# Kernel optimization log

Measured on AMD Instinct MI355X. Metric: run time of the kernel, lower is better.

The kernel has to match this reference:

```python
import jax, jax.numpy as jnp
import numpy as np

EMBED_DIM = 1024
NUM_HEADS = 16
HEAD_DIM = EMBED_DIM // NUM_HEADS
B, S = 2, 2048


def setup_inputs() -> dict:
    key = jax.random.key(0)
    ks = jax.random.split(key, 11)
    sc = 1.0 / np.sqrt(EMBED_DIM)
    d = {
        'query': jax.random.normal(ks[0], (B, S, EMBED_DIM), jnp.float32),
        'key': jax.random.normal(ks[1], (B, S, EMBED_DIM), jnp.float32),
        'value': jax.random.normal(ks[2], (B, S, EMBED_DIM), jnp.float32),
        'Wq': jax.random.normal(ks[3], (EMBED_DIM, EMBED_DIM), jnp.float32) * sc,
        'bq': jnp.zeros((EMBED_DIM,), jnp.float32),
        'Wk': jax.random.normal(ks[4], (EMBED_DIM, EMBED_DIM), jnp.float32) * sc,
        'bk': jnp.zeros((EMBED_DIM,), jnp.float32),
        'Wv': jax.random.normal(ks[5], (EMBED_DIM, EMBED_DIM), jnp.float32) * sc,
        'bv': jnp.zeros((EMBED_DIM,), jnp.float32),
        'Wo': jax.random.normal(ks[6], (EMBED_DIM, EMBED_DIM), jnp.float32) * sc,
        'bo': jnp.zeros((EMBED_DIM,), jnp.float32),
    }
    return d


def reference(query, key, value, Wq, bq, Wk, bk, Wv, bv, Wo, bo):
    b, s, _ = query.shape
    scale = 1.0 / np.sqrt(HEAD_DIM)
    # projections: torch Linear is x @ W.T + b
    q = (query @ Wq.T + bq).reshape(b, s, NUM_HEADS, HEAD_DIM).transpose(0, 2, 1, 3)
    k = (key @ Wk.T + bk).reshape(b, s, NUM_HEADS, HEAD_DIM).transpose(0, 2, 1, 3)
    v = (value @ Wv.T + bv).reshape(b, s, NUM_HEADS, HEAD_DIM).transpose(0, 2, 1, 3)
    scores = jnp.einsum('bhqd,bhkd->bhqk', q, k) * scale  # [B,H,S,S]
    causal = jnp.triu(jnp.ones((s, s), bool), k=1)
    scores = jnp.where(causal, -jnp.inf, scores)
    attn = jax.nn.softmax(scores, axis=-1)
    out = jnp.einsum('bhqk,bhkd->bhqd', attn, v)
    out = out.transpose(0, 2, 1, 3).reshape(b, s, EMBED_DIM)
    out = out @ Wo.T + bo
    return out, attn
```

## Files before the change

kernel.cpp:

```cpp
#include <hip/hip_runtime.h>
#include <hip/hip_bf16.h>

#define BATCH  2
#define SEQ    2048
#define EMBED  1024
#define NHEADS 16
#define HDIM   64
#define SCALE  0.125f
#define S2     0.180336880f
#define MFIX   20.0f
#define PPITCH 88

typedef __attribute__((ext_vector_type(8))) short   short8;
typedef __attribute__((ext_vector_type(4))) float   floatx4;

#if __has_builtin(__builtin_amdgcn_exp2f)
#define EXP2(x) __builtin_amdgcn_exp2f(x)
#else
#define EXP2(x) exp2f(x)
#endif

#define GLOAD_LDS(g, l) __builtin_amdgcn_global_load_lds(                      \
    (const __attribute__((address_space(1))) void*)(const void*)(g),           \
    (__attribute__((address_space(3))) void*)(void*)(l), 16, 0, 0)

__device__ __forceinline__ float bf2f(unsigned short h) {
    union { unsigned int u; float f; } v; v.u = ((unsigned int)h) << 16; return v.f;
}
__device__ __forceinline__ unsigned short f2bf(float f) {
    union { float f; unsigned int u; } v; v.f = f;
    unsigned int r = v.u + 0x7FFF + ((v.u >> 16) & 1);
    return (unsigned short)(r >> 16);
}
__device__ __forceinline__ unsigned int pack2(float lo, float hi) {
    return (unsigned int)f2bf(lo) | ((unsigned int)f2bf(hi) << 16);
}

__device__ __forceinline__ void bar_lds() {
    __builtin_amdgcn_sched_barrier(0);
    asm volatile("s_waitcnt lgkmcnt(0)" ::: "memory");
    __builtin_amdgcn_s_barrier();
    __builtin_amdgcn_sched_barrier(0);
}

__global__ __launch_bounds__(256)
void cvt_bf16(const float* __restrict__ q,  const float* __restrict__ k,
              const float* __restrict__ v,  const float* __restrict__ wq,
              const float* __restrict__ wk, const float* __restrict__ wv,
              const float* __restrict__ wo,
              unsigned short* __restrict__ dq,  unsigned short* __restrict__ dk,
              unsigned short* __restrict__ dv,  unsigned short* __restrict__ dwq,
              unsigned short* __restrict__ dwk, unsigned short* __restrict__ dwv,
              unsigned short* __restrict__ dwo)
{
    const float* s; unsigned short* d; int n;
    switch (blockIdx.y) {
        case 0: s = q;  d = dq;  n = BATCH * SEQ * EMBED; break;
        case 1: s = k;  d = dk;  n = BATCH * SEQ * EMBED; break;
        case 2: s = v;  d = dv;  n = BATCH * SEQ * EMBED; break;
        case 3: s = wq; d = dwq; n = EMBED * EMBED; break;
        case 4: s = wk; d = dwk; n = EMBED * EMBED; break;
        case 5: s = wv; d = dwv; n = EMBED * EMBED; break;
        default: s = wo; d = dwo; n = EMBED * EMBED; break;
    }
    const int i = (blockIdx.x * 256 + threadIdx.x) * 8;
    if (i >= n) return;
    float4 f0 = ((const float4*)(s + i))[0];
    float4 f1 = ((const float4*)(s + i))[1];
    uint4 u = {pack2(f0.x, f0.y), pack2(f0.z, f0.w),
               pack2(f1.x, f1.y), pack2(f1.z, f1.w)};
    *(uint4*)(d + i) = u;
}

__device__ __forceinline__ void gemm_body(
    const unsigned short* __restrict__ A,
    const unsigned short* __restrict__ W,
    const float* __restrict__ bias,
    void* __restrict__ Cout, const int f32out)
{
    constexpr int N = EMBED;
    constexpr int K = EMBED;

    __shared__ unsigned short As[2][128 * 64];
    __shared__ unsigned short Bs[2][64 * 64];

    const int t    = threadIdx.x;
    const int w    = t >> 6;
    const int lane = t & 63;
    const int lr   = lane & 15;
    const int quad = lane >> 4;
    const int n0   = blockIdx.x * 64;
    const int m0   = blockIdx.y * 128;

    size_t agoff[4];
    #pragma unroll
    for (int i = 0; i < 4; ++i) {
        const int slot = i * 256 + w * 64 + lane;
        const int row  = slot >> 3;
        const int g    = (slot & 7) ^ (row & 7);
        agoff[i] = (size_t)(m0 + row) * K + g * 8;
    }
    size_t bgoff[2];
    #pragma unroll
    for (int i = 0; i < 2; ++i) {
        const int slot = i * 256 + w * 64 + lane;
        const int row  = slot >> 3;
        const int g    = (slot & 7) ^ (row & 7);
        bgoff[i] = (size_t)(n0 + row) * K + g * 8;
    }

    int aoff[2][2], boff[4][2];
    #pragma unroll
    for (int mb = 0; mb < 2; ++mb)
        #pragma unroll
        for (int s = 0; s < 2; ++s) {
            const int row = w * 32 + mb * 16 + lr;
            aoff[mb][s] = row * 64 + (((s * 4 + quad) ^ (row & 7)) * 8);
        }
    #pragma unroll
    for (int nb = 0; nb < 4; ++nb)
        #pragma unroll
        for (int s = 0; s < 2; ++s) {
            const int row = nb * 16 + lr;
            boff[nb][s] = row * 64 + (((s * 4 + quad) ^ (row & 7)) * 8);
        }

    floatx4 acc[2][4];
    #pragma unroll
    for (int mb = 0; mb < 2; ++mb)
        #pragma unroll
        for (int nb = 0; nb < 4; ++nb) acc[mb][nb] = (floatx4){0.f, 0.f, 0.f, 0.f};

    auto stage = [&](int buf, int k0) {
        #pragma unroll
        for (int i = 0; i < 4; ++i)
            GLOAD_LDS(A + agoff[i] + k0, &As[buf][(i * 256 + w * 64) * 8]);
        #pragma unroll
        for (int i = 0; i < 2; ++i)
            GLOAD_LDS(W + bgoff[i] + k0, &Bs[buf][(i * 256 + w * 64) * 8]);
    };
    auto compute = [&](int buf) {
        const unsigned short* Ab = As[buf];
        const unsigned short* Bb = Bs[buf];
        #pragma unroll
        for (int s = 0; s < 2; ++s) {
            short8 a0 = *(const short8*)&Ab[aoff[0][s]];
            short8 a1 = *(const short8*)&Ab[aoff[1][s]];
            #pragma unroll
            for (int nb = 0; nb < 4; ++nb) {
                short8 bfr = *(const short8*)&Bb[boff[nb][s]];
                acc[0][nb] = __builtin_amdgcn_mfma_f32_16x16x32_bf16(a0, bfr, acc[0][nb], 0, 0, 0);
                acc[1][nb] = __builtin_amdgcn_mfma_f32_16x16x32_bf16(a1, bfr, acc[1][nb], 0, 0, 0);
            }
        }
    };

    stage(0, 0);
    __syncthreads();
    for (int k0 = 0; k0 < K; k0 += 128) {
        if (k0 + 64 < K) stage(1, k0 + 64);
        compute(0);
        __syncthreads();
        if (k0 + 128 < K) stage(0, k0 + 128);
        compute(1);
        __syncthreads();
    }

    #pragma unroll
    for (int mb = 0; mb < 2; ++mb)
        #pragma unroll
        for (int nb = 0; nb < 4; ++nb) {
            const int col = n0 + nb * 16 + lr;
            const float bv = bias[col];
            #pragma unroll
            for (int r = 0; r < 4; ++r) {
                const int row = m0 + w * 32 + mb * 16 + quad * 4 + r;
                const float val = acc[mb][nb][r] + bv;
                if (f32out) ((float*)Cout)[(size_t)row * N + col] = val;
                else        ((unsigned short*)Cout)[(size_t)row * N + col] = f2bf(val);
            }
        }
}

__global__ __launch_bounds__(256)
void gemm_qkv(const unsigned short* __restrict__ xq, const unsigned short* __restrict__ xk,
              const unsigned short* __restrict__ xv,
              const unsigned short* __restrict__ wq, const unsigned short* __restrict__ wk,
              const unsigned short* __restrict__ wv,
              const float* __restrict__ bq, const float* __restrict__ bk,
              const float* __restrict__ bv,
              unsigned short* __restrict__ Qb, unsigned short* __restrict__ Kb,
              unsigned short* __restrict__ Vb)
{
    const unsigned short *A, *W; const float* bias; unsigned short* C;
    switch (blockIdx.z) {
        case 0:  A = xq; W = wq; bias = bq; C = Qb; break;
        case 1:  A = xk; W = wk; bias = bk; C = Kb; break;
        default: A = xv; W = wv; bias = bv; C = Vb; break;
    }
    gemm_body(A, W, bias, C, 0);
}

__global__ __launch_bounds__(256)
void gemm_out(const unsigned short* __restrict__ A, const unsigned short* __restrict__ W,
              const float* __restrict__ bias, float* __restrict__ Cout)
{
    gemm_body(A, W, bias, Cout, 1);
}

__global__ __launch_bounds__(256)
void attn_fused(const unsigned short* __restrict__ Qb,
                const unsigned short* __restrict__ Kb,
                const unsigned short* __restrict__ Vb,
                float* __restrict__ attn,
                unsigned short* __restrict__ AO)
{
    __shared__ unsigned short Ps[64][PPITCH];
    __shared__ unsigned short Vt[2][64][PPITCH];

    const int t    = threadIdx.x;
    const int w    = t >> 6;
    const int lane = t & 63;
    const int lr   = lane & 15;
    const int quad = lane >> 4;
    const int h    = blockIdx.y;
    const int b    = blockIdx.z;
    const int slot = (h >> 3) + 2 * b;
    const int qt   = (slot & 1) ? (SEQ / 64 - 1 - (int)blockIdx.x) : (int)blockIdx.x;
    const int q0   = qt * 64;
    const int srow = t >> 2;
    const int sseg = (t & 3) * 16;

    const size_t kvbase = (size_t)b * SEQ * EMBED + h * HDIM;

    const unsigned short* qrow = Qb + kvbase + (size_t)(q0 + w * 16 + lr) * EMBED + quad * 8;
    const short8 af0 = *(const short8*)(qrow);
    const short8 af1 = *(const short8*)(qrow + 32);

    const unsigned short* kfrag = Kb + kvbase + (size_t)lr * EMBED + quad * 8;
    const unsigned short* Vrow  = Vb + kvbase + (size_t)lane * EMBED;

    float lsum[4];
    #pragma unroll
    for (int r = 0; r < 4; ++r) lsum[r] = 0.f;

    for (int kt = 0; kt <= qt; ++kt) {
        const unsigned short* kp = kfrag + (size_t)(kt * 64) * EMBED;
        short8 kb0[4], kb1[4];
        #pragma unroll
        for (int nb = 0; nb < 4; ++nb) kb0[nb] = *(const short8*)(kp + (size_t)(nb * 16) * EMBED);
        #pragma unroll
        for (int nb = 0; nb < 4; ++nb) kb1[nb] = *(const short8*)(kp + (size_t)(nb * 16) * EMBED + 32);

        floatx4 sf[4];
        #pragma unroll
        for (int i = 0; i < 4; ++i) sf[i] = (floatx4){0.f, 0.f, 0.f, 0.f};
        #pragma unroll
        for (int nb = 0; nb < 4; ++nb)
            sf[nb] = __builtin_amdgcn_mfma_f32_16x16x32_bf16(af0, kb0[nb], sf[nb], 0, 0, 0);
        #pragma unroll
        for (int nb = 0; nb < 4; ++nb)
            sf[nb] = __builtin_amdgcn_mfma_f32_16x16x32_bf16(af1, kb1[nb], sf[nb], 0, 0, 0);

        if (kt < qt) {
            #pragma unroll
            for (int r = 0; r < 4; ++r) {
                float e0 = EXP2(sf[0][r] * S2 - MFIX);
                float e1 = EXP2(sf[1][r] * S2 - MFIX);
                float e2 = EXP2(sf[2][r] * S2 - MFIX);
                float e3 = EXP2(sf[3][r] * S2 - MFIX);
                lsum[r] += (e0 + e1) + (e2 + e3);
            }
        } else {
            #pragma unroll
            for (int r = 0; r < 4; ++r) {
                const int q = w * 16 + quad * 4 + r;
                float e[4];
                #pragma unroll
                for (int nb = 0; nb < 4; ++nb) {
                    const int k = nb * 16 + lr;
                    float x = sf[nb][r] * S2 - MFIX;
                    if (k > q) x = -1e30f;
                    e[nb] = EXP2(x);
                }
                lsum[r] += (e[0] + e[1]) + (e[2] + e[3]);
            }
        }
    }

    float invl[4];
    #pragma unroll
    for (int r = 0; r < 4; ++r) {
        #pragma unroll
        for (int off = 1; off < 16; off <<= 1)
            lsum[r] += __shfl_xor(lsum[r], off, 64);
        invl[r] = 1.f / lsum[r];
    }

    floatx4 of[4];
    #pragma unroll
    for (int i = 0; i < 4; ++i) of[i] = (floatx4){0.f, 0.f, 0.f, 0.f};

    float* attn_bh = attn + ((size_t)(b * NHEADS + h)) * SEQ * SEQ;

    auto stageVt = [&](int buf, const uint4& a, const uint4& bb) {
        const unsigned short* pv0 = (const unsigned short*)&a;
        const unsigned short* pv1 = (const unsigned short*)&bb;
        #pragma unroll
        for (int j = 0; j < 8; ++j) Vt[buf][w * 8 + j][lane]       = pv0[j];
        #pragma unroll
        for (int j = 0; j < 8; ++j) Vt[buf][(w + 4) * 8 + j][lane] = pv1[j];
    };

    uint4 va  = *(const uint4*)(Vrow + w * 8);
    uint4 vb2 = *(const uint4*)(Vrow + (w + 4) * 8);
    stageVt(0, va, vb2);
    if (qt > 0) {
        va  = *(const uint4*)(Vrow + (size_t)64 * EMBED + w * 8);
        vb2 = *(const uint4*)(Vrow + (size_t)64 * EMBED + (w + 4) * 8);
    }
    bar_lds();

    for (int kt = 0; kt <= qt; ++kt) {
        const int k0 = kt * 64;

        const unsigned short* kp = kfrag + (size_t)k0 * EMBED;
        short8 kb0[4], kb1[4];
        #pragma unroll
        for (int nb = 0; nb < 4; ++nb) kb0[nb] = *(const short8*)(kp + (size_t)(nb * 16) * EMBED);
        #pragma unroll
        for (int nb = 0; nb < 4; ++nb) kb1[nb] = *(const short8*)(kp + (size_t)(nb * 16) * EMBED + 32);

        if (kt) bar_lds();

        if (kt < qt) {
            stageVt((kt + 1) & 1, va, vb2);
            if (kt + 2 <= qt) {
                va  = *(const uint4*)(Vrow + (size_t)(k0 + 128) * EMBED + w * 8);
                vb2 = *(const uint4*)(Vrow + (size_t)(k0 + 128) * EMBED + (w + 4) * 8);
            }
        }

        floatx4 sf[4];
        #pragma unroll
        for (int i = 0; i < 4; ++i) sf[i] = (floatx4){0.f, 0.f, 0.f, 0.f};
        #pragma unroll
        for (int nb = 0; nb < 4; ++nb)
            sf[nb] = __builtin_amdgcn_mfma_f32_16x16x32_bf16(af0, kb0[nb], sf[nb], 0, 0, 0);
        #pragma unroll
        for (int nb = 0; nb < 4; ++nb)
            sf[nb] = __builtin_amdgcn_mfma_f32_16x16x32_bf16(af1, kb1[nb], sf[nb], 0, 0, 0);

        if (kt < qt) {
            #pragma unroll
            for (int nb = 0; nb < 4; ++nb)
                #pragma unroll
                for (int r = 0; r < 4; ++r) {
                    float p = EXP2(sf[nb][r] * S2 - MFIX) * invl[r];
                    Ps[w * 16 + quad * 4 + r][nb * 16 + lr] = f2bf(p);
                }
        } else {
            #pragma unroll
            for (int nb = 0; nb < 4; ++nb) {
                const int k = nb * 16 + lr;
                #pragma unroll
                for (int r = 0; r < 4; ++r) {
                    const int q = w * 16 + quad * 4 + r;
                    float p = 0.f;
                    if (k <= q) p = EXP2(sf[nb][r] * S2 - MFIX) * invl[r];
                    Ps[w * 16 + quad * 4 + r][nb * 16 + lr] = f2bf(p);
                }
            }
        }

        {
            const int rrow = lane >> 2;
            const int rseg = (lane & 3) * 16;
            const unsigned short* ps = &Ps[w * 16 + rrow][rseg];
            float* op = attn_bh + (size_t)(q0 + w * 16 + rrow) * SEQ + k0 + rseg;
            #pragma unroll
            for (int g = 0; g < 4; ++g) {
                float4 f;
                f.x = bf2f(ps[g * 4 + 0]);
                f.y = bf2f(ps[g * 4 + 1]);
                f.z = bf2f(ps[g * 4 + 2]);
                f.w = bf2f(ps[g * 4 + 3]);
                ((float4*)op)[g] = f;
            }
        }

        #pragma unroll
        for (int s = 0; s < 2; ++s) {
            short8 paf = *(const short8*)&Ps[w * 16 + lr][s * 32 + quad * 8];
            #pragma unroll
            for (int nb = 0; nb < 4; ++nb) {
                short8 vf = *(const short8*)&Vt[kt & 1][nb * 16 + lr][s * 32 + quad * 8];
                of[nb] = __builtin_amdgcn_mfma_f32_16x16x32_bf16(paf, vf, of[nb], 0, 0, 0);
            }
        }
    }

    for (int kt = qt + 1; kt < SEQ / 64; ++kt) {
        float4 z = {0.f, 0.f, 0.f, 0.f};
        float* op = attn_bh + (size_t)(q0 + srow) * SEQ + kt * 64 + sseg;
        #pragma unroll
        for (int g = 0; g < 4; ++g) ((float4*)op)[g] = z;
    }

    #pragma unroll
    for (int nb = 0; nb < 4; ++nb)
        #pragma unroll
        for (int r = 0; r < 4; ++r)
            Ps[w * 16 + quad * 4 + r][nb * 16 + lr] = f2bf(of[nb][r]);
    {
        const int rrow = lane >> 2;
        const int rseg = (lane & 3) * 16;
        unsigned short* ao = AO + (size_t)(b * SEQ + q0 + w * 16 + rrow) * EMBED + h * HDIM + rseg;
        *(uint4*)ao       = *(const uint4*)&Ps[w * 16 + rrow][rseg];
        *(uint4*)(ao + 8) = *(const uint4*)&Ps[w * 16 + rrow][rseg + 8];
    }
}

extern "C" void kernel_launch(void* const* d_in, const int* in_sizes, int n_in,
                              void* d_out, int out_size, void* d_ws, size_t ws_size,
                              hipStream_t stream)
{
    const float* query = (const float*)d_in[0];
    const float* key   = (const float*)d_in[1];
    const float* value = (const float*)d_in[2];
    const float* Wq    = (const float*)d_in[3];
    const float* bq    = (const float*)d_in[4];
    const float* Wk    = (const float*)d_in[5];
    const float* bk    = (const float*)d_in[6];
    const float* Wv    = (const float*)d_in[7];
    const float* bv    = (const float*)d_in[8];
    const float* Wo    = (const float*)d_in[9];
    const float* bo    = (const float*)d_in[10];

    float* out  = (float*)d_out;
    float* attn = out + (size_t)BATCH * SEQ * EMBED;

    const size_t tsz = (size_t)BATCH * SEQ * EMBED;
    const size_t wsz = (size_t)EMBED * EMBED;
    unsigned short* p = (unsigned short*)d_ws;
    unsigned short* xq  = p;  p += tsz;
    unsigned short* xk  = p;  p += tsz;
    unsigned short* xv  = p;  p += tsz;
    unsigned short* wq16 = p; p += wsz;
    unsigned short* wk16 = p; p += wsz;
    unsigned short* wv16 = p; p += wsz;
    unsigned short* wo16 = p; p += wsz;
    unsigned short* Qb  = p;  p += tsz;
    unsigned short* Kb  = p;  p += tsz;
    unsigned short* Vb  = p;  p += tsz;
    unsigned short* AO  = p;  p += tsz;

    const dim3 blk(256);

    cvt_bf16<<<dim3(2048, 7), blk, 0, stream>>>(query, key, value, Wq, Wk, Wv, Wo,
                                                xq, xk, xv, wq16, wk16, wv16, wo16);

    const dim3 gqkv(EMBED / 64, (BATCH * SEQ) / 128, 3);
    gemm_qkv<<<gqkv, blk, 0, stream>>>(xq, xk, xv, wq16, wk16, wv16,
                                       bq, bk, bv, Qb, Kb, Vb);

    attn_fused<<<dim3(SEQ / 64, NHEADS, BATCH), blk, 0, stream>>>(Qb, Kb, Vb, attn, AO);

    const dim3 gout(EMBED / 64, (BATCH * SEQ) / 128);
    gemm_out<<<gout, blk, 0, stream>>>(AO, wo16, bo, out);
}
```

Measured before the change: 835.4 us.

## Single-pass attention with unnormalized bf16 probs, normalize in fused out-proj kernel

Removes the first pass that only computed row sums. A single pass now accumulates the softmax denominator while computing P·V, stages K tiles in shared memory with double buffering, and writes unnormalized bf16 probabilities in place into the attn output buffer. A second kernel merges the output projection GEMM with a normalization pass. That pass rescales each stored row by its inverse row sum, widens it to fp32 and zero-fills the masked region. This halves the QK^T work and overlaps the out-proj with the attn writes, at the cost of an extra read and write of the causal part of the attention matrix. It also relies on in-place aliasing, where each fp32 row overwrites bf16 data that was written at double row pitch.

```diff
diff --git a/kernel.cpp b/kernel.cpp
--- a/kernel.cpp
+++ b/kernel.cpp
@@ -9,7 +9,7 @@
 #define SCALE  0.125f
 #define S2     0.180336880f
 #define MFIX   20.0f
-#define PPITCH 88
+#define PPITCH 72
 
 typedef __attribute__((ext_vector_type(8))) short   short8;
 typedef __attribute__((ext_vector_type(4))) float   floatx4;
@@ -76,7 +76,8 @@
     const unsigned short* __restrict__ A,
     const unsigned short* __restrict__ W,
     const float* __restrict__ bias,
-    void* __restrict__ Cout, const int f32out)
+    void* __restrict__ Cout, const int f32out,
+    const int bx, const int by)
 {
     constexpr int N = EMBED;
     constexpr int K = EMBED;
@@ -89,8 +90,8 @@
     const int lane = t & 63;
     const int lr   = lane & 15;
     const int quad = lane >> 4;
-    const int n0   = blockIdx.x * 64;
-    const int m0   = blockIdx.y * 128;
+    const int n0   = bx * 64;
+    const int m0   = by * 128;
 
     size_t agoff[4];
     #pragma unroll
@@ -198,25 +199,20 @@
         case 1:  A = xk; W = wk; bias = bk; C = Kb; break;
         default: A = xv; W = wv; bias = bv; C = Vb; break;
     }
-    gemm_body(A, W, bias, C, 0);
+    gemm_body(A, W, bias, C, 0, blockIdx.x, blockIdx.y);
 }
 
 __global__ __launch_bounds__(256)
-void gemm_out(const unsigned short* __restrict__ A, const unsigned short* __restrict__ W,
-              const float* __restrict__ bias, float* __restrict__ Cout)
+void attn_pass(const unsigned short* __restrict__ Qb,
+               const unsigned short* __restrict__ Kb,
+               const unsigned short* __restrict__ Vb,
+               unsigned short* __restrict__ Pb,
+               float* __restrict__ Lbuf,
+               unsigned short* __restrict__ AO)
 {
-    gemm_body(A, W, bias, Cout, 1);
-}
-
-__global__ __launch_bounds__(256)
-void attn_fused(const unsigned short* __restrict__ Qb,
-                const unsigned short* __restrict__ Kb,
-                const unsigned short* __restrict__ Vb,
-                float* __restrict__ attn,
-                unsigned short* __restrict__ AO)
-{
+    __shared__ unsigned short Ks[2][64][PPITCH];
+    __shared__ unsigned short Vt[2][64][PPITCH];
     __shared__ unsigned short Ps[64][PPITCH];
-    __shared__ unsigned short Vt[2][64][PPITCH];
 
     const int t    = threadIdx.x;
     const int w    = t >> 6;
@@ -230,6 +226,7 @@
     const int q0   = qt * 64;
     const int srow = t >> 2;
     const int sseg = (t & 3) * 16;
+    const int bh   = b * NHEADS + h;
 
     const size_t kvbase = (size_t)b * SEQ * EMBED + h * HDIM;
 
@@ -237,126 +234,107 @@
     const short8 af0 = *(const short8*)(qrow);
     const short8 af1 = *(const short8*)(qrow + 32);
 
-    const unsigned short* kfrag = Kb + kvbase + (size_t)lr * EMBED + quad * 8;
-    const unsigned short* Vrow  = Vb + kvbase + (size_t)lane * EMBED;
+    const unsigned short* Krow = Kb + kvbase + (size_t)srow * EMBED + sseg;
+    const unsigned short* Vrow = Vb + kvbase + (size_t)lane * EMBED;
+
+    uint4 kA0, kA1, vA0, vA1;
+    uint4 kB0, kB1, vB0, vB1;
+
+    kA0 = ((const uint4*)Krow)[0];
+    kA1 = ((const uint4*)Krow)[1];
+    vA0 = *(const uint4*)(Vrow + w * 8);
+    vA1 = *(const uint4*)(Vrow + (w + 4) * 8);
+    *(uint4*)&Ks[0][srow][sseg]     = kA0;
+    *(uint4*)&Ks[0][srow][sseg + 8] = kA1;
+    {
+        const unsigned short* p0 = (const unsigned short*)&vA0;
+        const unsigned short* p1 = (const unsigned short*)&vA1;
+        #pragma unroll
+        for (int j = 0; j < 8; ++j) Vt[0][w * 8 + j][lane]       = p0[j];
+        #pragma unroll
+        for (int j = 0; j < 8; ++j) Vt[0][(w + 4) * 8 + j][lane] = p1[j];
+    }
+    if (qt > 0) {
+        const unsigned short* kp = Krow + (size_t)64 * EMBED;
+        kB0 = ((const uint4*)kp)[0];
+        kB1 = ((const uint4*)kp)[1];
+        vB0 = *(const uint4*)(Vrow + (size_t)64 * EMBED + w * 8);
+        vB1 = *(const uint4*)(Vrow + (size_t)64 * EMBED + (w + 4) * 8);
+    }
+    bar_lds();
 
     float lsum[4];
     #pragma unroll
     for (int r = 0; r < 4; ++r) lsum[r] = 0.f;
+    floatx4 of[4];
+    #pragma unroll
+    for (int i = 0; i < 4; ++i) of[i] = (floatx4){0.f, 0.f, 0.f, 0.f};
+
+    unsigned short* pb_bh = Pb + (size_t)bh * SEQ * (SEQ * 2);
+    const int rrow = lane >> 2;
+    const int rseg = (lane & 3) * 16;
 
     for (int kt = 0; kt <= qt; ++kt) {
-        const unsigned short* kp = kfrag + (size_t)(kt * 64) * EMBED;
-        short8 kb0[4], kb1[4];
-        #pragma unroll
-        for (int nb = 0; nb < 4; ++nb) kb0[nb] = *(const short8*)(kp + (size_t)(nb * 16) * EMBED);
-        #pragma unroll
-        for (int nb = 0; nb < 4; ++nb) kb1[nb] = *(const short8*)(kp + (size_t)(nb * 16) * EMBED + 32);
+        const int c  = kt & 1;
+        const int k0 = kt * 64;
+
+        if (kt < qt) {
+            if ((kt & 1) == 0) {
+                *(uint4*)&Ks[c ^ 1][srow][sseg]     = kB0;
+                *(uint4*)&Ks[c ^ 1][srow][sseg + 8] = kB1;
+                const unsigned short* p0 = (const unsigned short*)&vB0;
+                const unsigned short* p1 = (const unsigned short*)&vB1;
+                #pragma unroll
+                for (int j = 0; j < 8; ++j) Vt[c ^ 1][w * 8 + j][lane]       = p0[j];
+                #pragma unroll
+                for (int j = 0; j < 8; ++j) Vt[c ^ 1][(w + 4) * 8 + j][lane] = p1[j];
+                if (kt + 2 <= qt) {
+                    const unsigned short* kp = Krow + (size_t)(k0 + 128) * EMBED;
+                    kA0 = ((const uint4*)kp)[0];
+                    kA1 = ((const uint4*)kp)[1];
+                    vA0 = *(const uint4*)(Vrow + (size_t)(k0 + 128) * EMBED + w * 8);
+                    vA1 = *(const uint4*)(Vrow + (size_t)(k0 + 128) * EMBED + (w + 4) * 8);
+                }
+            } else {
+                *(uint4*)&Ks[c ^ 1][srow][sseg]     = kA0;
+                *(uint4*)&Ks[c ^ 1][srow][sseg + 8] = kA1;
+                const unsigned short* p0 = (const unsigned short*)&vA0;
+                const unsigned short* p1 = (const unsigned short*)&vA1;
+                #pragma unroll
+                for (int j = 0; j < 8; ++j) Vt[c ^ 1][w * 8 + j][lane]       = p0[j];
+                #pragma unroll
+                for (int j = 0; j < 8; ++j) Vt[c ^ 1][(w + 4) * 8 + j][lane] = p1[j];
+                if (kt + 2 <= qt) {
+                    const unsigned short* kp = Krow + (size_t)(k0 + 128) * EMBED;
+                    kB0 = ((const uint4*)kp)[0];
+                    kB1 = ((const uint4*)kp)[1];
+                    vB0 = *(const uint4*)(Vrow + (size_t)(k0 + 128) * EMBED + w * 8);
+                    vB1 = *(const uint4*)(Vrow + (size_t)(k0 + 128) * EMBED + (w + 4) * 8);
+                }
+            }
+        }
 
         floatx4 sf[4];
         #pragma unroll
         for (int i = 0; i < 4; ++i) sf[i] = (floatx4){0.f, 0.f, 0.f, 0.f};
         #pragma unroll
-        for (int nb = 0; nb < 4; ++nb)
-            sf[nb] = __builtin_amdgcn_mfma_f32_16x16x32_bf16(af0, kb0[nb], sf[nb], 0, 0, 0);
-        #pragma unroll
-        for (int nb = 0; nb < 4; ++nb)
-            sf[nb] = __builtin_amdgcn_mfma_f32_16x16x32_bf16(af1, kb1[nb], sf[nb], 0, 0, 0);
-
-        if (kt < qt) {
-            #pragma unroll
-            for (int r = 0; r < 4; ++r) {
-                float e0 = EXP2(sf[0][r] * S2 - MFIX);
-                float e1 = EXP2(sf[1][r] * S2 - MFIX);
-                float e2 = EXP2(sf[2][r] * S2 - MFIX);
-                float e3 = EXP2(sf[3][r] * S2 - MFIX);
-                lsum[r] += (e0 + e1) + (e2 + e3);
-            }
-        } else {
-            #pragma unroll
-            for (int r = 0; r < 4; ++r) {
-                const int q = w * 16 + quad * 4 + r;
-                float e[4];
-                #pragma unroll
-                for (int nb = 0; nb < 4; ++nb) {
-                    const int k = nb * 16 + lr;
-                    float x = sf[nb][r] * S2 - MFIX;
-                    if (k > q) x = -1e30f;
-                    e[nb] = EXP2(x);
-                }
-                lsum[r] += (e[0] + e[1]) + (e[2] + e[3]);
-            }
-        }
-    }
-
-    float invl[4];
-    #pragma unroll
-    for (int r = 0; r < 4; ++r) {
-        #pragma unroll
-        for (int off = 1; off < 16; off <<= 1)
-            lsum[r] += __shfl_xor(lsum[r], off, 64);
-        invl[r] = 1.f / lsum[r];
-    }
-
-    floatx4 of[4];
-    #pragma unroll
-    for (int i = 0; i < 4; ++i) of[i] = (floatx4){0.f, 0.f, 0.f, 0.f};
-
-    float* attn_bh = attn + ((size_t)(b * NHEADS + h)) * SEQ * SEQ;
-
-    auto stageVt = [&](int buf, const uint4& a, const uint4& bb) {
-        const unsigned short* pv0 = (const unsigned short*)&a;
-        const unsigned short* pv1 = (const unsigned short*)&bb;
-        #pragma unroll
-        for (int j = 0; j < 8; ++j) Vt[buf][w * 8 + j][lane]       = pv0[j];
-        #pragma unroll
-        for (int j = 0; j < 8; ++j) Vt[buf][(w + 4) * 8 + j][lane] = pv1[j];
-    };
-
-    uint4 va  = *(const uint4*)(Vrow + w * 8);
-    uint4 vb2 = *(const uint4*)(Vrow + (w + 4) * 8);
-    stageVt(0, va, vb2);
-    if (qt > 0) {
-        va  = *(const uint4*)(Vrow + (size_t)64 * EMBED + w * 8);
-        vb2 = *(const uint4*)(Vrow + (size_t)64 * EMBED + (w + 4) * 8);
-    }
-    bar_lds();
-
-    for (int kt = 0; kt <= qt; ++kt) {
-        const int k0 = kt * 64;
-
-        const unsigned short* kp = kfrag + (size_t)k0 * EMBED;
-        short8 kb0[4], kb1[4];
-        #pragma unroll
-        for (int nb = 0; nb < 4; ++nb) kb0[nb] = *(const short8*)(kp + (size_t)(nb * 16) * EMBED);
-        #pragma unroll
-        for (int nb = 0; nb < 4; ++nb) kb1[nb] = *(const short8*)(kp + (size_t)(nb * 16) * EMBED + 32);
-
-        if (kt) bar_lds();
-
-        if (kt < qt) {
-            stageVt((kt + 1) & 1, va, vb2);
-            if (kt + 2 <= qt) {
-                va  = *(const uint4*)(Vrow + (size_t)(k0 + 128) * EMBED + w * 8);
-                vb2 = *(const uint4*)(Vrow + (size_t)(k0 + 128) * EMBED + (w + 4) * 8);
-            }
-        }
-
-        floatx4 sf[4];
-        #pragma unroll
-        for (int i = 0; i < 4; ++i) sf[i] = (floatx4){0.f, 0.f, 0.f, 0.f};
-        #pragma unroll
-        for (int nb = 0; nb < 4; ++nb)
-            sf[nb] = __builtin_amdgcn_mfma_f32_16x16x32_bf16(af0, kb0[nb], sf[nb], 0, 0, 0);
-        #pragma unroll
-        for (int nb = 0; nb < 4; ++nb)
-            sf[nb] = __builtin_amdgcn_mfma_f32_16x16x32_bf16(af1, kb1[nb], sf[nb], 0, 0, 0);
+        for (int nb = 0; nb < 4; ++nb) {
+            short8 bf0 = *(const short8*)&Ks[c][nb * 16 + lr][quad * 8];
+            sf[nb] = __builtin_amdgcn_mfma_f32_16x16x32_bf16(af0, bf0, sf[nb], 0, 0, 0);
+        }
+        #pragma unroll
+        for (int nb = 0; nb < 4; ++nb) {
+            short8 bf1 = *(const short8*)&Ks[c][nb * 16 + lr][32 + quad * 8];
+            sf[nb] = __builtin_amdgcn_mfma_f32_16x16x32_bf16(af1, bf1, sf[nb], 0, 0, 0);
+        }
 
         if (kt < qt) {
             #pragma unroll
             for (int nb = 0; nb < 4; ++nb)
                 #pragma unroll
                 for (int r = 0; r < 4; ++r) {
-                    float p = EXP2(sf[nb][r] * S2 - MFIX) * invl[r];
+                    float p = EXP2(sf[nb][r] * S2 - MFIX);
+                    lsum[r] += p;
                     Ps[w * 16 + quad * 4 + r][nb * 16 + lr] = f2bf(p);
                 }
         } else {
@@ -367,57 +345,108 @@
                 for (int r = 0; r < 4; ++r) {
                     const int q = w * 16 + quad * 4 + r;
                     float p = 0.f;
-                    if (k <= q) p = EXP2(sf[nb][r] * S2 - MFIX) * invl[r];
+                    if (k <= q) { p = EXP2(sf[nb][r] * S2 - MFIX); lsum[r] += p; }
                     Ps[w * 16 + quad * 4 + r][nb * 16 + lr] = f2bf(p);
                 }
             }
         }
 
         {
-            const int rrow = lane >> 2;
-            const int rseg = (lane & 3) * 16;
             const unsigned short* ps = &Ps[w * 16 + rrow][rseg];
-            float* op = attn_bh + (size_t)(q0 + w * 16 + rrow) * SEQ + k0 + rseg;
-            #pragma unroll
-            for (int g = 0; g < 4; ++g) {
-                float4 f;
-                f.x = bf2f(ps[g * 4 + 0]);
-                f.y = bf2f(ps[g * 4 + 1]);
-                f.z = bf2f(ps[g * 4 + 2]);
-                f.w = bf2f(ps[g * 4 + 3]);
-                ((float4*)op)[g] = f;
-            }
-        }
-
-        #pragma unroll
-        for (int s = 0; s < 2; ++s) {
-            short8 paf = *(const short8*)&Ps[w * 16 + lr][s * 32 + quad * 8];
+            unsigned short* op = pb_bh + (size_t)(q0 + w * 16 + rrow) * (SEQ * 2) + k0 + rseg;
+            *(uint4*)op       = *(const uint4*)ps;
+            *(uint4*)(op + 8) = *(const uint4*)(ps + 8);
+        }
+
+        #pragma unroll
+        for (int ss = 0; ss < 2; ++ss) {
+            short8 paf = *(const short8*)&Ps[w * 16 + lr][ss * 32 + quad * 8];
             #pragma unroll
             for (int nb = 0; nb < 4; ++nb) {
-                short8 vf = *(const short8*)&Vt[kt & 1][nb * 16 + lr][s * 32 + quad * 8];
+                short8 vf = *(const short8*)&Vt[c][nb * 16 + lr][ss * 32 + quad * 8];
                 of[nb] = __builtin_amdgcn_mfma_f32_16x16x32_bf16(paf, vf, of[nb], 0, 0, 0);
             }
         }
-    }
-
-    for (int kt = qt + 1; kt < SEQ / 64; ++kt) {
-        float4 z = {0.f, 0.f, 0.f, 0.f};
-        float* op = attn_bh + (size_t)(q0 + srow) * SEQ + kt * 64 + sseg;
-        #pragma unroll
-        for (int g = 0; g < 4; ++g) ((float4*)op)[g] = z;
+
+        bar_lds();
+    }
+
+    float invl[4];
+    #pragma unroll
+    for (int r = 0; r < 4; ++r) {
+        #pragma unroll
+        for (int off = 1; off < 16; off <<= 1)
+            lsum[r] += __shfl_xor(lsum[r], off, 64);
+        invl[r] = 1.f / lsum[r];
+    }
+    if (lr == 0) {
+        #pragma unroll
+        for (int r = 0; r < 4; ++r)
+            Lbuf[(size_t)bh * SEQ + q0 + w * 16 + quad * 4 + r] = invl[r];
     }
 
     #pragma unroll
     for (int nb = 0; nb < 4; ++nb)
         #pragma unroll
         for (int r = 0; r < 4; ++r)
-            Ps[w * 16 + quad * 4 + r][nb * 16 + lr] = f2bf(of[nb][r]);
+            Ps[w * 16 + quad * 4 + r][nb * 16 + lr] = f2bf(of[nb][r] * invl[r]);
     {
-        const int rrow = lane >> 2;
-        const int rseg = (lane & 3) * 16;
         unsigned short* ao = AO + (size_t)(b * SEQ + q0 + w * 16 + rrow) * EMBED + h * HDIM + rseg;
         *(uint4*)ao       = *(const uint4*)&Ps[w * 16 + rrow][rseg];
         *(uint4*)(ao + 8) = *(const uint4*)&Ps[w * 16 + rrow][rseg + 8];
+    }
+}
+
+__global__ __launch_bounds__(256)
+void out_norm(const unsigned short* __restrict__ AO, const unsigned short* __restrict__ Wo16,
+              const float* __restrict__ bo, float* __restrict__ out,
+              float* __restrict__ attn, const float* __restrict__ Lbuf)
+{
+    const int id = blockIdx.x;
+    if (id < 512) {
+        gemm_body(AO, Wo16, bo, out, 1, id & 15, id >> 4);
+        return;
+    }
+    const int id2   = id - 512;
+    const int bh    = id2 >> 5;
+    const int x     = id2 & 31;
+    const int chunk = (bh & 1) ? (31 - x) : x;
+    const int t     = threadIdx.x;
+    const int w     = t >> 6;
+    const int lane  = t & 63;
+
+    const unsigned short* pb = (const unsigned short*)(attn + (size_t)bh * SEQ * SEQ);
+    float* ab = attn + (size_t)bh * SEQ * SEQ;
+
+    for (int i = 0; i < 16; ++i) {
+        const int q  = chunk * 64 + w * 16 + i;
+        const int qc = (q & ~63) + 64;
+        const float il = Lbuf[(size_t)bh * SEQ + q];
+        const unsigned short* src = pb + (size_t)q * (SEQ * 2);
+        float* dst = ab + (size_t)q * SEQ;
+
+        uint4 rr[4];
+        #pragma unroll
+        for (int s = 0; s < 4; ++s) {
+            const int c = lane * 8 + s * 512;
+            if (c < qc) rr[s] = *(const uint4*)(src + c);
+        }
+        #pragma unroll
+        for (int s = 0; s < 4; ++s) {
+            const int c = lane * 8 + s * 512;
+            if (c < qc) {
+                const unsigned short* u = (const unsigned short*)&rr[s];
+                float4 f0 = {bf2f(u[0]) * il, bf2f(u[1]) * il, bf2f(u[2]) * il, bf2f(u[3]) * il};
+                float4 f1 = {bf2f(u[4]) * il, bf2f(u[5]) * il, bf2f(u[6]) * il, bf2f(u[7]) * il};
+                ((float4*)(dst + c))[0] = f0;
+                ((float4*)(dst + c))[1] = f1;
+            }
+        }
+        for (int c = qc + lane * 8; c < SEQ; c += 512) {
+            float4 z = {0.f, 0.f, 0.f, 0.f};
+            ((float4*)(dst + c))[0] = z;
+            ((float4*)(dst + c))[1] = z;
+        }
     }
 }
 
@@ -455,6 +484,8 @@
     unsigned short* Vb  = p;  p += tsz;
     unsigned short* AO  = p;  p += tsz;
 
+    float* Lbuf = (float*)xq;
+
     const dim3 blk(256);
 
     cvt_bf16<<<dim3(2048, 7), blk, 0, stream>>>(query, key, value, Wq, Wk, Wv, Wo,
@@ -464,8 +495,8 @@
     gemm_qkv<<<gqkv, blk, 0, stream>>>(xq, xk, xv, wq16, wk16, wv16,
                                        bq, bk, bv, Qb, Kb, Vb);
 
-    attn_fused<<<dim3(SEQ / 64, NHEADS, BATCH), blk, 0, stream>>>(Qb, Kb, Vb, attn, AO);
-
-    const dim3 gout(EMBED / 64, (BATCH * SEQ) / 128);
-    gemm_out<<<gout, blk, 0, stream>>>(AO, wo16, bo, out);
-}
+    attn_pass<<<dim3(SEQ / 64, NHEADS, BATCH), blk, 0, stream>>>(
+        Qb, Kb, Vb, (unsigned short*)attn, Lbuf, AO);
+
+    out_norm<<<dim3(512 + 1024), blk, 0, stream>>>(AO, wo16, bo, out, attn, Lbuf);
+}
```

After: 832.0 us. No clear change (-0.4%).
